# Kernel optimization log

Hardware: AMD Instinct MI355X
Metric: run time of the kernel (lower is better)

The kernel has to match this reference:

```python
import jax, jax.numpy as jnp
import numpy as np

BETA = 0.25


def setup_inputs() -> dict:
    key = jax.random.key(0)
    k1, k2 = jax.random.split(key)
    x = jax.random.normal(k1, (32, 64, 64, 64), dtype=jnp.float32)   # [B, C, H, W]
    emb = jax.random.normal(k2, (1024, 64), dtype=jnp.float32)       # [K, C] codebook
    return {"x": x, "emb": emb}


def reference(x, emb):
    b, c, h, w = x.shape
    # (b h w) c
    z = jnp.transpose(x, (0, 2, 3, 1)).reshape(-1, c)
    # squared euclidean distances (argmin identical to torch.cdist argmin)
    # ||z||^2 - 2 z e^T + ||e||^2, never taking sqrt since only argmin is used
    d = (jnp.sum(z * z, axis=1, keepdims=True)
         - 2.0 * jnp.einsum('nc,kc->nk', z, emb)
         + jnp.sum(emb * emb, axis=1)[None, :])        # [N, K]
    idx = jnp.argmin(d, axis=1)                        # [N] int
    e = emb[idx]                                       # gather [N, C]
    e = jnp.transpose(e.reshape(b, h, w, c), (0, 3, 1, 2))  # [B, C, H, W]
    codebook_loss = jnp.mean((jax.lax.stop_gradient(x) - e) ** 2)
    commitment_loss = BETA * jnp.mean((x - jax.lax.stop_gradient(e)) ** 2)
    loss = codebook_loss + commitment_loss
    o = x + jax.lax.stop_gradient(e - x)               # straight-through
    indices = idx.reshape(b, h, w)
    return (o, loss, indices)
```

## Files before the change

kernel.cpp:

```cpp
#include <hip/hip_runtime.h>

#define BATCH   32
#define CCH     64
#define HW      4096
#define NPIX    131072
#define KCODES  1024
#define NELEM   (NPIX * CCH)
#define KSPLIT  4
#define CPB     256
#define PPB     1024
#define MARGIN_Q 2u

typedef _Float16 f16;
typedef __attribute__((ext_vector_type(8))) _Float16 f16x8;
typedef __attribute__((ext_vector_type(4))) _Float16 f16x4;
typedef __attribute__((ext_vector_type(4))) float    f32x4;

static __device__ __forceinline__ f32x4 mfma16(f16x8 a, f16x8 b, f32x4 c) {
    return __builtin_amdgcn_mfma_f32_16x16x32_f16(a, b, c, 0, 0, 0);
}

#define WS_PB1_U   1024
#define WS_PBG_B   (4096 + 4 * NPIX * 4)

__global__ __launch_bounds__(512, 2) void vq_main(
    const float* __restrict__ x, const float* __restrict__ emb,
    unsigned* __restrict__ pb1, unsigned char* __restrict__ pbg,
    float* __restrict__ wsf, unsigned* __restrict__ wsu)
{
    __shared__ __align__(16) f16 cbH[CPB * CCH];
    __shared__ __align__(16) f16 cbL[CPB * CCH];
    __shared__ float eebl[CPB];

    const int t    = threadIdx.x;
    const int lane = t & 63;
    const int w    = t >> 6;
    const int col  = lane & 15;
    const int quad = lane >> 4;
    const int c7   = col & 7;
    const int sw0  = 8 * (quad ^ c7);
    const int sw1  = sw0 ^ 32;
    const int gb   = blockIdx.x & 127;
    const int half = blockIdx.x >> 7;
    const int n0   = gb * PPB;
    const int b    = n0 >> 12;
    const int p0   = n0 & 4095;
    const int kbase = half * CPB;
    const float* xb = x + (size_t)b * (CCH * HW) + p0;
    const float* cb = emb + (size_t)kbase * CCH;

    if (blockIdx.x == 0 && t == 0) { wsf[0] = 0.f; wsu[1] = 0u; }

    {
        const float4* src = (const float4*)cb;
#pragma unroll
        for (int i = 0; i < 8; ++i) {
            const int j = i * 512 + t;
            float4 v = src[j];
            const int code = j >> 4, ch4 = j & 15;
            f16x4 h = {(f16)v.x, (f16)v.y, (f16)v.z, (f16)v.w};
            f16x4 l = {(f16)(v.x - (float)h[0]), (f16)(v.y - (float)h[1]),
                       (f16)(v.z - (float)h[2]), (f16)(v.w - (float)h[3])};
            const int off = code * 64 + 8 * ((ch4 >> 1) ^ (code & 7)) + (ch4 & 1) * 4;
            *(f16x4*)&cbH[off] = h;
            *(f16x4*)&cbL[off] = l;
        }
        if (t < CPB) {
            const float4* row4 = (const float4*)(cb + (size_t)t * CCH);
            float s = 0.f;
#pragma unroll
            for (int i = 0; i < 16; ++i) {
                float4 v = row4[i];
                s = fmaf(v.x, v.x, s); s = fmaf(v.y, v.y, s);
                s = fmaf(v.z, v.z, s); s = fmaf(v.w, v.w, s);
            }
            eebl[t] = fmaf(s, 2048.0f, 1048576.0f);
        }
    }
    __syncthreads();

    for (int it = 0; it < PPB / 512; ++it) {
        f16x8 aH[4][2], aL[4][2];
#pragma unroll
        for (int rt = 0; rt < 4; ++rt) {
            const int pp = it * 512 + w * 64 + rt * 16 + col;
#pragma unroll
            for (int kc = 0; kc < 2; ++kc) {
                f16x8 h, l;
#pragma unroll
                for (int j = 0; j < 8; ++j) {
                    const int c = kc * 32 + quad * 8 + j;
                    float zs = -2.0f * xb[(size_t)c * HW + pp];
                    f16 hh = (f16)zs;
                    h[j] = hh;
                    l[j] = (f16)(zs - (float)hh);
                }
                aH[rt][kc] = h;
                aL[rt][kc] = l;
            }
        }

        unsigned best[16], best2[16];
#pragma unroll
        for (int s = 0; s < 16; ++s) { best[s] = 0xFFFFFFFFu; best2[s] = 0xFFFFFFFFu; }

#pragma unroll 4
        for (int tile = 0; tile < CPB / 16; ++tile) {
            const int row = tile * 16 + col;
            const f16* bh = cbH + row * 64;
            const f16* bl = cbL + row * 64;
            f16x8 bH0 = *(const f16x8*)(bh + sw0);
            f16x8 bH1 = *(const f16x8*)(bh + sw1);
            f16x8 bL0 = *(const f16x8*)(bl + sw0);
            f16x8 bL1 = *(const f16x8*)(bl + sw1);
            const float eebc = eebl[row];
            const unsigned kb = (unsigned)(kbase + row);
#pragma unroll
            for (int rt = 0; rt < 4; ++rt) {
                f32x4 a4 = {0.f, 0.f, 0.f, 0.f};
                a4 = mfma16(aH[rt][0], bH0, a4);
                a4 = mfma16(aH[rt][1], bH1, a4);
                a4 = mfma16(aL[rt][0], bH0, a4);
                a4 = mfma16(aL[rt][1], bH1, a4);
                a4 = mfma16(aH[rt][0], bL0, a4);
                a4 = mfma16(aH[rt][1], bL1, a4);
#pragma unroll
                for (int r = 0; r < 4; ++r) {
                    float uf = fmaf(a4[r], 2048.0f, eebc);
                    unsigned pk = (((unsigned)uf) << 10) | kb;
                    const int s = rt * 4 + r;
                    best2[s] = min(best2[s], max(pk, best[s]));
                    best[s]  = min(best[s], pk);
                }
            }
        }

#pragma unroll
        for (int d = 1; d < 16; d <<= 1) {
#pragma unroll
            for (int s = 0; s < 16; ++s) {
                unsigned ob  = __shfl_xor(best[s],  d, 64);
                unsigned ob2 = __shfl_xor(best2[s], d, 64);
                best2[s] = min(min(best2[s], ob2), max(best[s], ob));
                best[s]  = min(best[s], ob);
            }
        }
        if (col == 0) {
            const unsigned baseN = (unsigned)(half * NPIX + n0 + it * 512 + w * 64);
#pragma unroll
            for (int rt = 0; rt < 4; ++rt)
#pragma unroll
                for (int r = 0; r < 4; ++r) {
                    const unsigned idx = baseN + rt * 16 + quad * 4 + r;
                    const unsigned bb = best[rt * 4 + r];
                    unsigned qg = (best2[rt * 4 + r] >> 10) - (bb >> 10);
                    pb1[idx] = bb;
                    pbg[idx] = (unsigned char)min(qg, 255u);
                }
        }
    }
}

__global__ __launch_bounds__(256) void vq_post(
    const float* __restrict__ x, const float* __restrict__ emb,
    const unsigned* __restrict__ pb1, const unsigned char* __restrict__ pbg,
    float* __restrict__ o, float* __restrict__ idx_out,
    float* __restrict__ loss_out, float* __restrict__ acc,
    unsigned* __restrict__ done)
{
    __shared__ float wred[4];
    __shared__ unsigned amb[256];
    __shared__ unsigned ambn;
    __shared__ float zsh[CCH];
    __shared__ double rbd[4];
    __shared__ int rbi[4];
    __shared__ int s_pk;
    __shared__ float s_extra;

    const int t = threadIdx.x, lane = t & 63, w = t >> 6;
    const int n = blockIdx.x * 256 + t;
    const int b = n >> 12, p = n & 4095;
    if (t == 0) { ambn = 0u; s_extra = 0.f; }
    __syncthreads();

    const unsigned b0 = pb1[n], b1 = pb1[NPIX + n];
    const unsigned b2 = pb1[2 * NPIX + n], b3 = pb1[3 * NPIX + n];
    const unsigned m1 = min(b0, b1), M1 = max(b0, b1);
    const unsigned m2 = min(b2, b3), M2 = max(b2, b3);
    const unsigned bu = min(m1, m2);
    const unsigned sb = min(max(m1, m2), min(M1, M2));
    const unsigned gsel = (bu == b0) ? pbg[n] : (bu == b1) ? pbg[NPIX + n]
                        : (bu == b2) ? pbg[2 * NPIX + n] : pbg[3 * NPIX + n];
    const unsigned bidx = bu & 1023u;
    idx_out[n] = (float)bidx;
    const unsigned qb = bu >> 10;
    const unsigned qsec = min(sb >> 10, qb + gsel);
    if (qsec - qb < MARGIN_Q) { unsigned pos = atomicAdd(&ambn, 1u); amb[pos] = (unsigned)t; }

    float ss = 0.f;
    {
        const float4* er4 = (const float4*)(emb + (size_t)bidx * CCH);
        const float* xbt = x + (size_t)b * (CCH * HW) + p;
        float* ob = o + (size_t)b * (CCH * HW) + p;
#pragma unroll
        for (int i = 0; i < 16; ++i) {
            float4 ev = er4[i];
            float evv[4] = {ev.x, ev.y, ev.z, ev.w};
#pragma unroll
            for (int q = 0; q < 4; ++q) {
                const int c = i * 4 + q;
                float xv = xbt[(size_t)c * HW];
                float e  = evv[q];
                ob[(size_t)c * HW] = xv + (e - xv);
                float d = xv - e;
                ss = fmaf(d, d, ss);
            }
        }
    }
    for (int off = 32; off; off >>= 1) ss += __shfl_down(ss, off, 64);
    if (lane == 0) wred[w] = ss;
    __syncthreads();

    unsigned cnt = ambn; if (cnt > 256u) cnt = 256u;
    for (unsigned u2 = 0; u2 < cnt; ++u2) {
        const int nn = blockIdx.x * 256 + (int)amb[u2];
        const int bb2 = nn >> 12, pp2 = nn & 4095;
        if (t < CCH) zsh[t] = x[(size_t)bb2 * (CCH * HW) + (size_t)t * HW + pp2];
        __syncthreads();

        double bd = 1e300; int bi = KCODES;
        for (int j = 0; j < 4; ++j) {
            const int k = t + j * 256;
            const float* er = emb + (size_t)k * CCH;
            double d0 = 0.0, d1 = 0.0, d2 = 0.0, d3 = 0.0;
#pragma unroll
            for (int c = 0; c < CCH; c += 4) {
                double t0 = (double)zsh[c + 0] - (double)er[c + 0];
                double t1 = (double)zsh[c + 1] - (double)er[c + 1];
                double t2 = (double)zsh[c + 2] - (double)er[c + 2];
                double t3 = (double)zsh[c + 3] - (double)er[c + 3];
                d0 = fma(t0, t0, d0); d1 = fma(t1, t1, d1);
                d2 = fma(t2, t2, d2); d3 = fma(t3, t3, d3);
            }
            double d = (d0 + d1) + (d2 + d3);
            if (d < bd) { bd = d; bi = k; }
        }
        for (int dlt = 1; dlt < 64; dlt <<= 1) {
            double od = __shfl_xor(bd, dlt, 64);
            int    oi = __shfl_xor(bi, dlt, 64);
            if (od < bd || (od == bd && oi < bi)) { bd = od; bi = oi; }
        }
        if (lane == 0) { rbd[w] = bd; rbi[w] = bi; }
        __syncthreads();
        if (t == 0) {
            double fb = rbd[0]; int fi = rbi[0];
            for (int q = 1; q < 4; ++q)
                if (rbd[q] < fb || (rbd[q] == fb && rbi[q] < fi)) { fb = rbd[q]; fi = rbi[q]; }
            const int old = (int)idx_out[nn];
            if (fi != old) { idx_out[nn] = (float)fi; s_pk = (old << 16) | fi; }
            else s_pk = -1;
        }
        __syncthreads();
        const int pk = s_pk;
        if (t < 64) {
            float delta = 0.f;
            if (pk >= 0) {
                const int old = pk >> 16, fi = pk & 0xFFFF;
                const float xv = zsh[t];
                const float eo = emb[(size_t)old * CCH + t];
                const float en = emb[(size_t)fi  * CCH + t];
                o[(size_t)bb2 * (CCH * HW) + (size_t)t * HW + pp2] = xv + (en - xv);
                const float dn = xv - en, dd = xv - eo;
                delta = dn * dn - dd * dd;
            }
            for (int off = 32; off; off >>= 1) delta += __shfl_down(delta, off, 64);
            if (t == 0) s_extra += delta;
        }
        __syncthreads();
    }

    if (t == 0) {
        float tot = (wred[0] + wred[1]) + (wred[2] + wred[3]) + s_extra;
        atomicAdd(acc, tot);
        __threadfence();
        unsigned old = atomicAdd(done, 1u);
        if (old == gridDim.x - 1) {
            __threadfence();
            float fin = atomicAdd(acc, 0.f);
            loss_out[0] = 1.25f * fin * (1.0f / (float)NELEM);
        }
    }
}

extern "C" void kernel_launch(void* const* d_in, const int* in_sizes, int n_in,
                              void* d_out, int out_size, void* d_ws, size_t ws_size,
                              hipStream_t stream) {
    const float* x   = (const float*)d_in[0];
    const float* emb = (const float*)d_in[1];
    float*    out = (float*)d_out;
    float*    wsf = (float*)d_ws;
    unsigned* wsu = (unsigned*)d_ws;
    char*     wsb = (char*)d_ws;

    float* o_out    = out;
    float* loss_out = out + NELEM;
    float* idx_out  = out + NELEM + 1;
    unsigned*      pb1 = wsu + WS_PB1_U;
    unsigned char* pbg = (unsigned char*)(wsb + WS_PBG_B);

    vq_main<<<(NPIX / PPB) * KSPLIT, 512, 0, stream>>>(x, emb, pb1, pbg, wsf, wsu);
    vq_post<<<NPIX / 256, 256, 0, stream>>>(x, emb, pb1, pbg, o_out, idx_out,
                                            loss_out, wsf, wsu + 1);
}
```

Before: 188.1 us.

## Fuse VQ distance search and epilogue into one kernel with full-codebook blocks

Replaces the K-split main kernel plus post kernel with a single fused kernel. Each 512-pixel block now scans the whole codebook in two shared-memory halves, keeping the A fragments in registers. It then writes indices and outputs directly and handles near-tie pixels with a per-wave fp64 recheck. This removes the global round trip of the per-split best/gap buffers and the global atomic loss reduction, which a tiny finishing kernel replaces. Grid size drops to 256 blocks and each block reloads the codebook twice, so parallelism and codebook reuse shift. It also uses v_med3 for second-best tracking.

```diff
diff --git a/kernel.cpp b/kernel.cpp
--- a/kernel.cpp
+++ b/kernel.cpp
@@ -1,111 +1,102 @@
 #include <hip/hip_runtime.h>
 
-#define BATCH   32
 #define CCH     64
 #define HW      4096
 #define NPIX    131072
 #define KCODES  1024
 #define NELEM   (NPIX * CCH)
-#define KSPLIT  4
-#define CPB     256
-#define PPB     1024
+#define PPB     512
+#define HALFK   512
 #define MARGIN_Q 2u
 
 typedef _Float16 f16;
 typedef __attribute__((ext_vector_type(8))) _Float16 f16x8;
-typedef __attribute__((ext_vector_type(4))) _Float16 f16x4;
 typedef __attribute__((ext_vector_type(4))) float    f32x4;
 
 static __device__ __forceinline__ f32x4 mfma16(f16x8 a, f16x8 b, f32x4 c) {
     return __builtin_amdgcn_mfma_f32_16x16x32_f16(a, b, c, 0, 0, 0);
 }
-
-#define WS_PB1_U   1024
-#define WS_PBG_B   (4096 + 4 * NPIX * 4)
-
-__global__ __launch_bounds__(512, 2) void vq_main(
+static __device__ __forceinline__ unsigned med3u(unsigned a, unsigned b, unsigned c) {
+    unsigned d;
+    asm("v_med3_u32 %0, %1, %2, %3" : "=v"(d) : "v"(a), "v"(b), "v"(c));
+    return d;
+}
+
+__global__ __launch_bounds__(512, 2) void vq_fused(
     const float* __restrict__ x, const float* __restrict__ emb,
-    unsigned* __restrict__ pb1, unsigned char* __restrict__ pbg,
-    float* __restrict__ wsf, unsigned* __restrict__ wsu)
+    float* __restrict__ o, float* __restrict__ idx_out,
+    float* __restrict__ partial)
 {
-    __shared__ __align__(16) f16 cbH[CPB * CCH];
-    __shared__ __align__(16) f16 cbL[CPB * CCH];
-    __shared__ float eebl[CPB];
+    __shared__ __align__(16) f16 cbH[HALFK * CCH];
+    __shared__ __align__(16) f16 cbL[HALFK * CCH];
+    __shared__ float eebl[HALFK];
+    __shared__ unsigned buS[PPB];
+    __shared__ float wred[8];
 
     const int t    = threadIdx.x;
     const int lane = t & 63;
     const int w    = t >> 6;
     const int col  = lane & 15;
     const int quad = lane >> 4;
-    const int c7   = col & 7;
-    const int sw0  = 8 * (quad ^ c7);
+    const int sw0  = 8 * (quad ^ (col & 7));
     const int sw1  = sw0 ^ 32;
-    const int gb   = blockIdx.x & 127;
-    const int half = blockIdx.x >> 7;
-    const int n0   = gb * PPB;
+    const int n0   = blockIdx.x * PPB;
     const int b    = n0 >> 12;
     const int p0   = n0 & 4095;
-    const int kbase = half * CPB;
     const float* xb = x + (size_t)b * (CCH * HW) + p0;
-    const float* cb = emb + (size_t)kbase * CCH;
-
-    if (blockIdx.x == 0 && t == 0) { wsf[0] = 0.f; wsu[1] = 0u; }
-
-    {
-        const float4* src = (const float4*)cb;
-#pragma unroll
-        for (int i = 0; i < 8; ++i) {
-            const int j = i * 512 + t;
-            float4 v = src[j];
-            const int code = j >> 4, ch4 = j & 15;
-            f16x4 h = {(f16)v.x, (f16)v.y, (f16)v.z, (f16)v.w};
-            f16x4 l = {(f16)(v.x - (float)h[0]), (f16)(v.y - (float)h[1]),
-                       (f16)(v.z - (float)h[2]), (f16)(v.w - (float)h[3])};
-            const int off = code * 64 + 8 * ((ch4 >> 1) ^ (code & 7)) + (ch4 & 1) * 4;
-            *(f16x4*)&cbH[off] = h;
-            *(f16x4*)&cbL[off] = l;
-        }
-        if (t < CPB) {
-            const float4* row4 = (const float4*)(cb + (size_t)t * CCH);
+
+    f16x8 aH[4][2], aL[4][2];
+#pragma unroll
+    for (int rt = 0; rt < 4; ++rt) {
+        const int pp = w * 64 + rt * 16 + col;
+#pragma unroll
+        for (int kc = 0; kc < 2; ++kc) {
+            f16x8 h, l;
+#pragma unroll
+            for (int j = 0; j < 8; ++j) {
+                const int c = kc * 32 + quad * 8 + j;
+                float zs = -2.0f * xb[(size_t)c * HW + pp];
+                f16 hh = (f16)zs;
+                h[j] = hh;
+                l[j] = (f16)(zs - (float)hh);
+            }
+            aH[rt][kc] = h;
+            aL[rt][kc] = l;
+        }
+    }
+
+    unsigned best[16], best2[16];
+#pragma unroll
+    for (int s = 0; s < 16; ++s) { best[s] = 0xFFFFFFFFu; best2[s] = 0xFFFFFFFFu; }
+
+    for (int half = 0; half < 2; ++half) {
+        const int kbase = half * HALFK;
+        {
+            const float* src = emb + (size_t)(kbase + t) * CCH;
             float s = 0.f;
 #pragma unroll
-            for (int i = 0; i < 16; ++i) {
-                float4 v = row4[i];
-                s = fmaf(v.x, v.x, s); s = fmaf(v.y, v.y, s);
-                s = fmaf(v.z, v.z, s); s = fmaf(v.w, v.w, s);
+            for (int g = 0; g < 8; ++g) {
+                float4 v0 = *(const float4*)(src + g * 8);
+                float4 v1 = *(const float4*)(src + g * 8 + 4);
+                float vv[8] = {v0.x, v0.y, v0.z, v0.w, v1.x, v1.y, v1.z, v1.w};
+                f16x8 h, l;
+#pragma unroll
+                for (int j = 0; j < 8; ++j) {
+                    f16 hh = (f16)vv[j];
+                    h[j] = hh;
+                    l[j] = (f16)(vv[j] - (float)hh);
+                    s = fmaf(vv[j], vv[j], s);
+                }
+                const int off = t * 64 + 8 * (g ^ (t & 7));
+                *(f16x8*)&cbH[off] = h;
+                *(f16x8*)&cbL[off] = l;
             }
             eebl[t] = fmaf(s, 2048.0f, 1048576.0f);
         }
-    }
-    __syncthreads();
-
-    for (int it = 0; it < PPB / 512; ++it) {
-        f16x8 aH[4][2], aL[4][2];
-#pragma unroll
-        for (int rt = 0; rt < 4; ++rt) {
-            const int pp = it * 512 + w * 64 + rt * 16 + col;
-#pragma unroll
-            for (int kc = 0; kc < 2; ++kc) {
-                f16x8 h, l;
-#pragma unroll
-                for (int j = 0; j < 8; ++j) {
-                    const int c = kc * 32 + quad * 8 + j;
-                    float zs = -2.0f * xb[(size_t)c * HW + pp];
-                    f16 hh = (f16)zs;
-                    h[j] = hh;
-                    l[j] = (f16)(zs - (float)hh);
-                }
-                aH[rt][kc] = h;
-                aL[rt][kc] = l;
-            }
-        }
-
-        unsigned best[16], best2[16];
-#pragma unroll
-        for (int s = 0; s < 16; ++s) { best[s] = 0xFFFFFFFFu; best2[s] = 0xFFFFFFFFu; }
+        __syncthreads();
 
 #pragma unroll 4
-        for (int tile = 0; tile < CPB / 16; ++tile) {
+        for (int tile = 0; tile < HALFK / 16; ++tile) {
             const int row = tile * 16 + col;
             const f16* bh = cbH + row * 64;
             const f16* bl = cbL + row * 64;
@@ -129,79 +120,46 @@
                     float uf = fmaf(a4[r], 2048.0f, eebc);
                     unsigned pk = (((unsigned)uf) << 10) | kb;
                     const int s = rt * 4 + r;
-                    best2[s] = min(best2[s], max(pk, best[s]));
+                    best2[s] = med3u(pk, best[s], best2[s]);
                     best[s]  = min(best[s], pk);
                 }
             }
         }
-
-#pragma unroll
-        for (int d = 1; d < 16; d <<= 1) {
-#pragma unroll
-            for (int s = 0; s < 16; ++s) {
-                unsigned ob  = __shfl_xor(best[s],  d, 64);
-                unsigned ob2 = __shfl_xor(best2[s], d, 64);
-                best2[s] = min(min(best2[s], ob2), max(best[s], ob));
-                best[s]  = min(best[s], ob);
-            }
-        }
-        if (col == 0) {
-            const unsigned baseN = (unsigned)(half * NPIX + n0 + it * 512 + w * 64);
-#pragma unroll
-            for (int rt = 0; rt < 4; ++rt)
-#pragma unroll
-                for (int r = 0; r < 4; ++r) {
-                    const unsigned idx = baseN + rt * 16 + quad * 4 + r;
-                    const unsigned bb = best[rt * 4 + r];
-                    unsigned qg = (best2[rt * 4 + r] >> 10) - (bb >> 10);
-                    pb1[idx] = bb;
-                    pbg[idx] = (unsigned char)min(qg, 255u);
-                }
-        }
-    }
-}
-
-__global__ __launch_bounds__(256) void vq_post(
-    const float* __restrict__ x, const float* __restrict__ emb,
-    const unsigned* __restrict__ pb1, const unsigned char* __restrict__ pbg,
-    float* __restrict__ o, float* __restrict__ idx_out,
-    float* __restrict__ loss_out, float* __restrict__ acc,
-    unsigned* __restrict__ done)
-{
-    __shared__ float wred[4];
-    __shared__ unsigned amb[256];
-    __shared__ unsigned ambn;
-    __shared__ float zsh[CCH];
-    __shared__ double rbd[4];
-    __shared__ int rbi[4];
-    __shared__ int s_pk;
-    __shared__ float s_extra;
-
-    const int t = threadIdx.x, lane = t & 63, w = t >> 6;
-    const int n = blockIdx.x * 256 + t;
-    const int b = n >> 12, p = n & 4095;
-    if (t == 0) { ambn = 0u; s_extra = 0.f; }
+        __syncthreads();
+    }
+
+#pragma unroll
+    for (int d = 1; d < 16; d <<= 1) {
+#pragma unroll
+        for (int s = 0; s < 16; ++s) {
+            unsigned ob  = __shfl_xor(best[s],  d, 64);
+            unsigned ob2 = __shfl_xor(best2[s], d, 64);
+            best2[s] = med3u(best[s], ob, min(best2[s], ob2));
+            best[s]  = min(best[s], ob);
+        }
+    }
+    if (col == 0) {
+#pragma unroll
+        for (int rt = 0; rt < 4; ++rt)
+#pragma unroll
+            for (int r = 0; r < 4; ++r) {
+                const int s = rt * 4 + r;
+                const unsigned bb = best[s];
+                const unsigned fl =
+                    (((best2[s] >> 10) - (bb >> 10)) < MARGIN_Q) ? 0x80000000u : 0u;
+                buS[w * 64 + rt * 16 + quad * 4 + r] = bb | fl;
+            }
+    }
     __syncthreads();
 
-    const unsigned b0 = pb1[n], b1 = pb1[NPIX + n];
-    const unsigned b2 = pb1[2 * NPIX + n], b3 = pb1[3 * NPIX + n];
-    const unsigned m1 = min(b0, b1), M1 = max(b0, b1);
-    const unsigned m2 = min(b2, b3), M2 = max(b2, b3);
-    const unsigned bu = min(m1, m2);
-    const unsigned sb = min(max(m1, m2), min(M1, M2));
-    const unsigned gsel = (bu == b0) ? pbg[n] : (bu == b1) ? pbg[NPIX + n]
-                        : (bu == b2) ? pbg[2 * NPIX + n] : pbg[3 * NPIX + n];
+    const unsigned bu = buS[t];
     const unsigned bidx = bu & 1023u;
-    idx_out[n] = (float)bidx;
-    const unsigned qb = bu >> 10;
-    const unsigned qsec = min(sb >> 10, qb + gsel);
-    if (qsec - qb < MARGIN_Q) { unsigned pos = atomicAdd(&ambn, 1u); amb[pos] = (unsigned)t; }
-
+    idx_out[n0 + t] = (float)bidx;
     float ss = 0.f;
     {
         const float4* er4 = (const float4*)(emb + (size_t)bidx * CCH);
-        const float* xbt = x + (size_t)b * (CCH * HW) + p;
-        float* ob = o + (size_t)b * (CCH * HW) + p;
+        const float* xbt = xb + t;
+        float* ob = o + (size_t)b * (CCH * HW) + p0 + t;
 #pragma unroll
         for (int i = 0; i < 16; ++i) {
             float4 ev = er4[i];
@@ -218,31 +176,35 @@
         }
     }
     for (int off = 32; off; off >>= 1) ss += __shfl_down(ss, off, 64);
-    if (lane == 0) wred[w] = ss;
-    __syncthreads();
-
-    unsigned cnt = ambn; if (cnt > 256u) cnt = 256u;
-    for (unsigned u2 = 0; u2 < cnt; ++u2) {
-        const int nn = blockIdx.x * 256 + (int)amb[u2];
-        const int bb2 = nn >> 12, pp2 = nn & 4095;
-        if (t < CCH) zsh[t] = x[(size_t)bb2 * (CCH * HW) + (size_t)t * HW + pp2];
-        __syncthreads();
-
-        double bd = 1e300; int bi = KCODES;
-        for (int j = 0; j < 4; ++j) {
-            const int k = t + j * 256;
-            const float* er = emb + (size_t)k * CCH;
-            double d0 = 0.0, d1 = 0.0, d2 = 0.0, d3 = 0.0;
-#pragma unroll
-            for (int c = 0; c < CCH; c += 4) {
-                double t0 = (double)zsh[c + 0] - (double)er[c + 0];
-                double t1 = (double)zsh[c + 1] - (double)er[c + 1];
-                double t2 = (double)zsh[c + 2] - (double)er[c + 2];
-                double t3 = (double)zsh[c + 3] - (double)er[c + 3];
+
+    unsigned long long flags = __ballot((bu >> 31) != 0u);
+    float extra = 0.f;
+    while (flags) {
+        const int m = __ffsll((long long)flags) - 1;
+        flags &= flags - 1;
+        const int pp2 = p0 + w * 64 + m;
+        const int n   = n0 + w * 64 + m;
+        const float zval = x[(size_t)b * (CCH * HW) + (size_t)lane * HW + pp2];
+        float zf[CCH];
+#pragma unroll
+        for (int c = 0; c < CCH; ++c) zf[c] = __shfl(zval, c, 64);
+
+        double bd = 1e300; int bi = 0;
+        for (int j = 0; j < 16; ++j) {
+            const int k = lane * 16 + j;
+            const float4* er4 = (const float4*)(emb + (size_t)k * CCH);
+            double d0 = 0.0, d1 = 0.0;
+#pragma unroll
+            for (int i = 0; i < 16; ++i) {
+                float4 ev = er4[i];
+                double t0 = (double)zf[i * 4 + 0] - (double)ev.x;
+                double t1 = (double)zf[i * 4 + 1] - (double)ev.y;
+                double t2 = (double)zf[i * 4 + 2] - (double)ev.z;
+                double t3 = (double)zf[i * 4 + 3] - (double)ev.w;
                 d0 = fma(t0, t0, d0); d1 = fma(t1, t1, d1);
-                d2 = fma(t2, t2, d2); d3 = fma(t3, t3, d3);
-            }
-            double d = (d0 + d1) + (d2 + d3);
+                d0 = fma(t2, t2, d0); d1 = fma(t3, t3, d1);
+            }
+            double d = d0 + d1;
             if (d < bd) { bd = d; bi = k; }
         }
         for (int dlt = 1; dlt < 64; dlt <<= 1) {
@@ -250,46 +212,38 @@
             int    oi = __shfl_xor(bi, dlt, 64);
             if (od < bd || (od == bd && oi < bi)) { bd = od; bi = oi; }
         }
-        if (lane == 0) { rbd[w] = bd; rbi[w] = bi; }
-        __syncthreads();
-        if (t == 0) {
-            double fb = rbd[0]; int fi = rbi[0];
-            for (int q = 1; q < 4; ++q)
-                if (rbd[q] < fb || (rbd[q] == fb && rbi[q] < fi)) { fb = rbd[q]; fi = rbi[q]; }
-            const int old = (int)idx_out[nn];
-            if (fi != old) { idx_out[nn] = (float)fi; s_pk = (old << 16) | fi; }
-            else s_pk = -1;
-        }
-        __syncthreads();
-        const int pk = s_pk;
-        if (t < 64) {
-            float delta = 0.f;
-            if (pk >= 0) {
-                const int old = pk >> 16, fi = pk & 0xFFFF;
-                const float xv = zsh[t];
-                const float eo = emb[(size_t)old * CCH + t];
-                const float en = emb[(size_t)fi  * CCH + t];
-                o[(size_t)bb2 * (CCH * HW) + (size_t)t * HW + pp2] = xv + (en - xv);
-                const float dn = xv - en, dd = xv - eo;
-                delta = dn * dn - dd * dd;
-            }
+        const int oldi = (int)(buS[w * 64 + m] & 1023u);
+        if (bi != oldi) {
+            if (lane == 0) idx_out[n] = (float)bi;
+            const float xv = zval;
+            const float eo = emb[(size_t)oldi * CCH + lane];
+            const float en = emb[(size_t)bi   * CCH + lane];
+            o[(size_t)b * (CCH * HW) + (size_t)lane * HW + pp2] = xv + (en - xv);
+            const float dn = xv - en, dd = xv - eo;
+            float delta = dn * dn - dd * dd;
             for (int off = 32; off; off >>= 1) delta += __shfl_down(delta, off, 64);
-            if (t == 0) s_extra += delta;
-        }
-        __syncthreads();
-    }
-
+            extra += delta;
+        }
+    }
+
+    if (lane == 0) wred[w] = ss + extra;
+    __syncthreads();
     if (t == 0) {
-        float tot = (wred[0] + wred[1]) + (wred[2] + wred[3]) + s_extra;
-        atomicAdd(acc, tot);
-        __threadfence();
-        unsigned old = atomicAdd(done, 1u);
-        if (old == gridDim.x - 1) {
-            __threadfence();
-            float fin = atomicAdd(acc, 0.f);
-            loss_out[0] = 1.25f * fin * (1.0f / (float)NELEM);
-        }
-    }
+        float tot = 0.f;
+#pragma unroll
+        for (int i = 0; i < 8; ++i) tot += wred[i];
+        partial[blockIdx.x] = tot;
+    }
+}
+
+__global__ void vq_fin(const float* __restrict__ partial, float* __restrict__ loss) {
+    __shared__ float r[4];
+    const int t = threadIdx.x, lane = t & 63, w = t >> 6;
+    float s = partial[t];
+    for (int off = 32; off; off >>= 1) s += __shfl_down(s, off, 64);
+    if (lane == 0) r[w] = s;
+    __syncthreads();
+    if (t == 0) loss[0] = 1.25f * ((r[0] + r[1]) + (r[2] + r[3])) * (1.0f / (float)NELEM);
 }
 
 extern "C" void kernel_launch(void* const* d_in, const int* in_sizes, int n_in,
@@ -297,18 +251,13 @@
                               hipStream_t stream) {
     const float* x   = (const float*)d_in[0];
     const float* emb = (const float*)d_in[1];
-    float*    out = (float*)d_out;
-    float*    wsf = (float*)d_ws;
-    unsigned* wsu = (unsigned*)d_ws;
-    char*     wsb = (char*)d_ws;
+    float* out = (float*)d_out;
+    float* wsf = (float*)d_ws;
 
     float* o_out    = out;
     float* loss_out = out + NELEM;
     float* idx_out  = out + NELEM + 1;
-    unsigned*      pb1 = wsu + WS_PB1_U;
-    unsigned char* pbg = (unsigned char*)(wsb + WS_PBG_B);
-
-    vq_main<<<(NPIX / PPB) * KSPLIT, 512, 0, stream>>>(x, emb, pb1, pbg, wsf, wsu);
-    vq_post<<<NPIX / 256, 256, 0, stream>>>(x, emb, pb1, pbg, o_out, idx_out,
-                                            loss_out, wsf, wsu + 1);
-}
+
+    vq_fused<<<NPIX / PPB, PPB, 0, stream>>>(x, emb, o_out, idx_out, wsf);
+    vq_fin<<<1, 256, 0, stream>>>(wsf, loss_out);
+}
```

Result: faster. 177.8 us (-5.5%).
